# Kernel tuning notes

Hardware: AMD Instinct MI355X
Metric: run time of the kernel (lower is better)

## Reference

```python
import jax, jax.numpy as jnp
import numpy as np

HID = 96
B = 64
PF = (HID + 1) ** 3  # 912673


def setup_inputs() -> dict:
    key = jax.random.key(0)
    ks = jax.random.split(key, 6)
    s1 = 1.0 / np.sqrt(PF)
    s2 = 1.0 / np.sqrt(HID)
    s3 = 1.0 / np.sqrt(HID // 2)
    return {
        "text_x": jax.random.normal(ks[0], (B, HID), jnp.float32),
        "audio_x": jax.random.normal(ks[1], (B, HID), jnp.float32),
        "video_x": jax.random.normal(ks[2], (B, HID), jnp.float32),
        "W1": jax.random.normal(ks[3], (HID, PF), jnp.float32) * s1,
        "b1": jnp.zeros((HID,), jnp.float32),
        "W2": jax.random.normal(ks[4], (HID // 2, HID), jnp.float32) * s2,
        "b2": jnp.zeros((HID // 2,), jnp.float32),
        "W3": jax.random.normal(ks[5], (3, HID // 2), jnp.float32) * s3,
        "b3": jnp.zeros((3,), jnp.float32),
    }


def reference(text_x, audio_x, video_x, W1, b1, W2, b2, W3, b3):
    bsz = text_x.shape[0]
    ones = jnp.ones((bsz, 1), text_x.dtype)
    t = jnp.concatenate([ones, text_x], axis=1)   # [B, H+1]
    a = jnp.concatenate([ones, audio_x], axis=1)  # [B, H+1]
    v = jnp.concatenate([ones, video_x], axis=1)  # [B, H+1]
    # outer product of the three modalities, flattened: [B, (H+1)^3]
    fusion = jnp.einsum("bi,bj,bk->bijk", t, a, v).reshape(bsz, -1)
    # post-fusion MLP (dropout is identity at inference)
    h = jax.nn.relu(fusion @ W1.T + b1)
    h = jax.nn.relu(h @ W2.T + b2)
    return h @ W3.T + b3
```

## Files before the change

### kernel.cpp

```cpp
#include <hip/hip_runtime.h>
#include <stdint.h>


#define HID   96
#define NP1   97
#define ROWLEN 9409
#define NBLK  9312
#define BATCH 64

typedef short bf16x8 __attribute__((ext_vector_type(8)));
typedef float f32x4  __attribute__((ext_vector_type(4)));

__device__ __forceinline__ short f2bf(float x) {
    union { float f; uint32_t u; } c; c.f = x;
    uint32_t r = (c.u + 0x7FFFu + ((c.u >> 16) & 1u)) >> 16;
    return (short)(uint16_t)r;
}

__global__ __launch_bounds__(256)
void fusion_gemm(const float* __restrict__ W1,
                 const float* __restrict__ text_x,
                 const float* __restrict__ audio_x,
                 const float* __restrict__ video_x,
                 float* __restrict__ h1pre)
{
    __shared__ __align__(16) float Ws[9416];
    const int tid = threadIdx.x;
    const int blk = blockIdx.x;
    const int o = blk / 97;
    const int i = blk - o * 97;

    const long tile_start = (long)blk * ROWLEN;
    const int  shift = (int)(tile_start & 3);
    const float4* Wg4 = reinterpret_cast<const float4*>(W1 + (tile_start - shift));
#pragma unroll
    for (int it = 0; it < 9; ++it) {
        int idx = it * 256 + tid;
        *reinterpret_cast<float4*>(&Ws[idx << 2]) = Wg4[idx];
    }
    {
        int idx = 2304 + tid;
        if (idx < 2353) *reinterpret_cast<float4*>(&Ws[idx << 2]) = Wg4[idx];
    }

    const int lane = tid & 63;
    const int wave = tid >> 6;
    const int quad = lane >> 4;
    const int col  = lane & 15;
    const int b    = wave * 16 + col;

    bf16x8 bfrag[3];
#pragma unroll
    for (int ks = 0; ks < 3; ++ks) {
        const float* vp = video_x + b * HID + ks * 32 + quad * 8;
        float4 v0 = *reinterpret_cast<const float4*>(vp);
        float4 v1 = *reinterpret_cast<const float4*>(vp + 4);
        bf16x8 f;
        f[0]=f2bf(v0.x); f[1]=f2bf(v0.y); f[2]=f2bf(v0.z); f[3]=f2bf(v0.w);
        f[4]=f2bf(v1.x); f[5]=f2bf(v1.y); f[6]=f2bf(v1.z); f[7]=f2bf(v1.w);
        bfrag[ks] = f;
    }

    __syncthreads();

    f32x4 acc[7];
#pragma unroll
    for (int mt = 0; mt < 7; ++mt) acc[mt] = (f32x4){0.f, 0.f, 0.f, 0.f};

#pragma unroll
    for (int ks = 0; ks < 3; ++ks) {
#pragma unroll
        for (int mt = 0; mt < 7; ++mt) {
            int j  = mt * 16 + col;
            int je = j > 96 ? 96 : j;
            const float* ap = &Ws[shift + je * NP1 + 1 + ks * 32 + quad * 8];
            bf16x8 af;
#pragma unroll
            for (int e = 0; e < 8; ++e) af[e] = f2bf(ap[e]);
            acc[mt] = __builtin_amdgcn_mfma_f32_16x16x32_bf16(af, bfrag[ks], acc[mt], 0, 0, 0);
        }
    }

    float s = 0.f;
#pragma unroll
    for (int mt = 0; mt < 7; ++mt) {
#pragma unroll
        for (int r = 0; r < 4; ++r) {
            int j = mt * 16 + quad * 4 + r;
            if (j < 97) {
                float u  = acc[mt][r] + Ws[shift + j * NP1];
                float aw = (j == 0) ? 1.f : audio_x[b * HID + (j - 1)];
                s += u * aw;
            }
        }
    }
    s += __shfl_xor(s, 16);
    s += __shfl_xor(s, 32);

    if (quad == 0) {
        float tw = (i == 0) ? 1.f : text_x[b * HID + (i - 1)];
        atomicAdd(&h1pre[o * BATCH + b], s * tw);
    }
}

__global__ __launch_bounds__(64)
void mlp_tail(const float* __restrict__ h1pre, const float* __restrict__ b1,
              const float* __restrict__ W2, const float* __restrict__ b2,
              const float* __restrict__ W3, const float* __restrict__ b3,
              float* __restrict__ out)
{
    __shared__ float h1s[96];
    __shared__ float h2s[48];
    const int b = blockIdx.x;
    const int t = threadIdx.x;
    for (int o = t; o < 96; o += 64) {
        float v = h1pre[o * BATCH + b] + b1[o];
        h1s[o] = v > 0.f ? v : 0.f;
    }
    __syncthreads();
    if (t < 48) {
        float acc = b2[t];
#pragma unroll 8
        for (int o = 0; o < 96; ++o) acc += W2[t * 96 + o] * h1s[o];
        h2s[t] = acc > 0.f ? acc : 0.f;
    }
    __syncthreads();
    if (t < 3) {
        float acc = b3[t];
#pragma unroll
        for (int c = 0; c < 48; ++c) acc += W3[t * 48 + c] * h2s[c];
        out[b * 3 + t] = acc;
    }
}

extern "C" void kernel_launch(void* const* d_in, const int* in_sizes, int n_in,
                              void* d_out, int out_size, void* d_ws, size_t ws_size,
                              hipStream_t stream)
{
    const float* text  = (const float*)d_in[0];
    const float* audio = (const float*)d_in[1];
    const float* video = (const float*)d_in[2];
    const float* W1    = (const float*)d_in[3];
    const float* b1    = (const float*)d_in[4];
    const float* W2    = (const float*)d_in[5];
    const float* b2    = (const float*)d_in[6];
    const float* W3    = (const float*)d_in[7];
    const float* b3    = (const float*)d_in[8];
    float* h1pre = (float*)d_ws;

    hipMemsetAsync(h1pre, 0, HID * BATCH * sizeof(float), stream);
    fusion_gemm<<<NBLK, 256, 0, stream>>>(W1, text, audio, video, h1pre);
    mlp_tail<<<BATCH, 64, 0, stream>>>(h1pre, b1, W2, b2, W3, b3, (float*)d_out);
}
```

Measured before the change: 522.9 us.

## Convert W1 tile to bf16 once when staging it into shared memory

```diff
diff --git a/kernel.cpp b/kernel.cpp
--- a/kernel.cpp
+++ b/kernel.cpp
@@ -2,45 +2,51 @@
 #include <stdint.h>
 
 
-#define HID   96
-#define NP1   97
+#define HID    96
+#define NP1    97
 #define ROWLEN 9409
-#define NBLK  9312
-#define BATCH 64
+#define NBLK   9312
+#define BATCH  64
+#define RSTR   104
 
 typedef short bf16x8 __attribute__((ext_vector_type(8)));
 typedef float f32x4  __attribute__((ext_vector_type(4)));
 
-__device__ __forceinline__ short f2bf(float x) {
-    union { float f; uint32_t u; } c; c.f = x;
-    uint32_t r = (c.u + 0x7FFFu + ((c.u >> 16) & 1u)) >> 16;
-    return (short)(uint16_t)r;
+__device__ __forceinline__ uint32_t pack2bf(float lo, float hi) {
+    union { float f; uint32_t u; } a, b; a.f = lo; b.f = hi;
+    uint32_t ra = (a.u + 0x7fffu + ((a.u >> 16) & 1u)) >> 16;
+    uint32_t rb = (b.u + 0x7fffu + ((b.u >> 16) & 1u)) & 0xffff0000u;
+    return ra | rb;
 }
 
-__global__ __launch_bounds__(256)
+__global__ __launch_bounds__(256, 6)
 void fusion_gemm(const float* __restrict__ W1,
                  const float* __restrict__ text_x,
                  const float* __restrict__ audio_x,
                  const float* __restrict__ video_x,
                  float* __restrict__ h1pre)
 {
-    __shared__ __align__(16) float Ws[9416];
+    __shared__ __align__(16) short Wbf[NP1 * RSTR];
+    __shared__ float biasF[NP1];
+
     const int tid = threadIdx.x;
     const int blk = blockIdx.x;
     const int o = blk / 97;
     const int i = blk - o * 97;
+    const float* Wt = W1 + (long)blk * ROWLEN;
 
-    const long tile_start = (long)blk * ROWLEN;
-    const int  shift = (int)(tile_start & 3);
-    const float4* Wg4 = reinterpret_cast<const float4*>(W1 + (tile_start - shift));
-#pragma unroll
-    for (int it = 0; it < 9; ++it) {
-        int idx = it * 256 + tid;
-        *reinterpret_cast<float4*>(&Ws[idx << 2]) = Wg4[idx];
-    }
-    {
-        int idx = 2304 + tid;
-        if (idx < 2353) *reinterpret_cast<float4*>(&Ws[idx << 2]) = Wg4[idx];
+    for (int j = tid; j < NP1; j += 256) biasF[j] = Wt[j * NP1];
+
+    for (int w = tid; w < NP1 * 12; w += 256) {
+        int j = w / 12;
+        int s = w - j * 12;
+        const float* p = Wt + j * NP1 + 1 + s * 8;
+        uint4 q;
+        q.x = pack2bf(p[0], p[1]);
+        q.y = pack2bf(p[2], p[3]);
+        q.z = pack2bf(p[4], p[5]);
+        q.w = pack2bf(p[6], p[7]);
+        *reinterpret_cast<uint4*>(&Wbf[j * RSTR + s * 8]) = q;
     }
 
     const int lane = tid & 63;
@@ -53,12 +59,12 @@
 #pragma unroll
     for (int ks = 0; ks < 3; ++ks) {
         const float* vp = video_x + b * HID + ks * 32 + quad * 8;
-        float4 v0 = *reinterpret_cast<const float4*>(vp);
-        float4 v1 = *reinterpret_cast<const float4*>(vp + 4);
-        bf16x8 f;
-        f[0]=f2bf(v0.x); f[1]=f2bf(v0.y); f[2]=f2bf(v0.z); f[3]=f2bf(v0.w);
-        f[4]=f2bf(v1.x); f[5]=f2bf(v1.y); f[6]=f2bf(v1.z); f[7]=f2bf(v1.w);
-        bfrag[ks] = f;
+        union { bf16x8 v; uint32_t d[4]; } u;
+        u.d[0] = pack2bf(vp[0], vp[1]);
+        u.d[1] = pack2bf(vp[2], vp[3]);
+        u.d[2] = pack2bf(vp[4], vp[5]);
+        u.d[3] = pack2bf(vp[6], vp[7]);
+        bfrag[ks] = u.v;
     }
 
     __syncthreads();
@@ -73,10 +79,7 @@
         for (int mt = 0; mt < 7; ++mt) {
             int j  = mt * 16 + col;
             int je = j > 96 ? 96 : j;
-            const float* ap = &Ws[shift + je * NP1 + 1 + ks * 32 + quad * 8];
-            bf16x8 af;
-#pragma unroll
-            for (int e = 0; e < 8; ++e) af[e] = f2bf(ap[e]);
+            bf16x8 af = *reinterpret_cast<const bf16x8*>(&Wbf[je * RSTR + ks * 32 + quad * 8]);
             acc[mt] = __builtin_amdgcn_mfma_f32_16x16x32_bf16(af, bfrag[ks], acc[mt], 0, 0, 0);
         }
     }
@@ -88,7 +91,7 @@
         for (int r = 0; r < 4; ++r) {
             int j = mt * 16 + quad * 4 + r;
             if (j < 97) {
-                float u  = acc[mt][r] + Ws[shift + j * NP1];
+                float u  = acc[mt][r] + biasF[j];
                 float aw = (j == 0) ? 1.f : audio_x[b * HID + (j - 1)];
                 s += u * aw;
             }
```

Result: slower. 539.9 us (+3.2%).
